# Kernel tuning notes

Measured on AMD Instinct MI355X. Metric: run time of the kernel, lower is better.

The kernel has to match this reference:

```python
import jax, jax.numpy as jnp
import numpy as np

N, C, T, H, W = 2, 512, 8, 28, 28
THW = T * H * W
BN_EPS = 1e-5


def conv1x1(x, Wt, b):
    # pointwise channel mixing, equivalent to 1x1 Conv2d/Conv3d on (N,C,T,H,W)
    return jnp.einsum('oc,ncthw->nothw', Wt, x) + b[None, :, None, None, None]


def setup_inputs() -> dict:
    key = jax.random.key(0)
    ks = jax.random.split(key, 8)
    s = 1.0 / np.sqrt(C)
    x = jax.random.normal(ks[0], (N, C, T, H, W), dtype=jnp.float32)
    mask = jax.random.uniform(ks[1], (N, C, T, H, W), dtype=jnp.float32)
    Wh = jax.random.normal(ks[2], (C, C), dtype=jnp.float32) * s
    Wg = jax.random.normal(ks[3], (C, C), dtype=jnp.float32) * s
    Wm = jax.random.normal(ks[4], (C, C), dtype=jnp.float32) * s
    Wz = jax.random.normal(ks[5], (C, C), dtype=jnp.float32) * s  # kaiming-like
    bh = jnp.zeros((C,), jnp.float32)
    bg = jnp.zeros((C,), jnp.float32)
    bm = jnp.zeros((C,), jnp.float32)
    bz = jnp.zeros((C,), jnp.float32)
    bn_w = jnp.ones((C,), jnp.float32)
    bn_b = jnp.zeros((C,), jnp.float32)
    gamma = jnp.float32(1.0)  # self.gamma (undefined in source __init__); learnable scalar
    return dict(x=x, mask=mask, Wh=Wh, bh=bh, Wg=Wg, bg=bg, Wm=Wm, bm=bm,
                Wz=Wz, bz=bz, bn_w=bn_w, bn_b=bn_b, gamma=gamma)


def reference(x, mask, Wh, bh, Wg, bg, Wm, bm, Wz, bz, bn_w, bn_b, gamma):
    n = x.shape[0]
    # proj_f = h(x) reshaped (N, THW, C); proj_g = g(x) (N, C, THW)
    ph_x = conv1x1(x, Wh, bh).reshape(n, C, THW)
    pg = conv1x1(x, Wg, bg).reshape(n, C, THW)
    # energy[n,t,s] = sum_c ph_x[n,c,t] * pg[n,c,s]  -> (N, THW, THW)
    energy = jnp.einsum('nct,ncs->nts', ph_x, pg)
    attention = jax.nn.softmax(energy, axis=-1)
    # proj_h uses self.h on mask (faithful to source)
    ph_m = conv1x1(mask, Wh, bh).reshape(n, C, THW)
    # bmm(proj_h, attention^T): [n,c,t] = sum_s ph_m[n,c,s] * attention[n,t,s]
    mask_energy = jnp.einsum('ncs,nts->nct', ph_m, attention)
    mask_atten = jax.nn.softmax(mask_energy, axis=-1)  # softmax over THW
    pm = conv1x1(x, Wm, bm)
    out = pm * mask_atten.reshape(n, C, T, H, W)
    # W_z: 1x1 Conv3d + BatchNorm3d (training-mode batch stats, weight=1, bias=0)
    wy = conv1x1(x, Wz, bz)
    mu = jnp.mean(wy, axis=(0, 2, 3, 4), keepdims=True)
    var = jnp.var(wy, axis=(0, 2, 3, 4), keepdims=True)
    wy = (wy - mu) * jax.lax.rsqrt(var + BN_EPS)
    wy = wy * bn_w[None, :, None, None, None] + bn_b[None, :, None, None, None]
    return gamma * out + wy
```

## Files before the change

### kernel.cpp

```cpp
#include <hip/hip_runtime.h>
#include <hip/hip_bf16.h>
#include <math.h>

#define NN 2
#define CC 512
#define PP 6272
#define TCHMAX 1664
#define NCHK 4
#define NJT 49
#define EM 64.0f
static const size_t PPC = (size_t)PP * CC;
static const size_t NCP = (size_t)NN * PPC;

typedef unsigned short ushortT;
typedef __attribute__((ext_vector_type(8))) short short8;
typedef __attribute__((ext_vector_type(4))) float f32x4;

__device__ __forceinline__ ushortT f2bf(float f) {
  __hip_bfloat16 h = __float2bfloat16(f);
  return *reinterpret_cast<ushortT*>(&h);
}
__device__ __forceinline__ float bf2f(ushortT u) {
  return __uint_as_float(((unsigned)u) << 16);
}

__device__ __forceinline__ void ld_g2l(const void* g, void* l) {
  __builtin_amdgcn_global_load_lds(
      (const __attribute__((address_space(1))) void*)g,
      (__attribute__((address_space(3))) void*)l, 16, 0, 0);
}

__device__ __forceinline__ int xcd_remap(int orig, int nwg) {
  const int q = nwg >> 3, r = nwg & 7;
  const int x = orig & 7, lo = orig >> 3;
  return (x < r) ? x * (q + 1) + lo : r * (q + 1) + (x - r) * q + lo;
}


__global__ __launch_bounds__(256) void k_cast4(const float* __restrict__ W0,
                                               const float* __restrict__ W1,
                                               const float* __restrict__ W2,
                                               const float* __restrict__ W3,
                                               ushortT* __restrict__ dst) {
  const float* src = (blockIdx.y == 0) ? W0 : (blockIdx.y == 1) ? W1
                    : (blockIdx.y == 2) ? W2 : W3;
  const int i = (blockIdx.x * 256 + threadIdx.x) * 4;
  float4 v = *(const float4*)&src[i];
  ushort4 o;
  o.x = f2bf(v.x); o.y = f2bf(v.y); o.z = f2bf(v.z); o.w = f2bf(v.w);
  *(ushort4*)&dst[(size_t)blockIdx.y * CC * CC + i] = o;
}

__global__ void k_castT2(const float* __restrict__ x,
                         const float* __restrict__ mask,
                         ushortT* __restrict__ xT,
                         ushortT* __restrict__ maskT) {
  __shared__ float T[32][33];
  const int zz = blockIdx.z;
  const float* in = (zz < 2) ? x : mask;
  ushortT* out = (zz < 2) ? xT : maskT;
  const int p0 = blockIdx.x * 32, c0 = blockIdx.y * 32;
  const int tx = threadIdx.x, ty = threadIdx.y;
  const size_t nbi = (size_t)(zz & 1) * PPC;
#pragma unroll
  for (int i = 0; i < 4; ++i)
    T[ty + i * 8][tx] = in[nbi + (size_t)(c0 + ty + i * 8) * PP + p0 + tx];
  __syncthreads();
#pragma unroll
  for (int i = 0; i < 4; ++i) {
    int r = ty + i * 8;
    out[nbi + (size_t)(p0 + r) * CC + c0 + tx] = f2bf(T[tx][r]);
  }
}

__global__ __launch_bounds__(256, 3) void k_convs(
    const ushortT* __restrict__ xT, const ushortT* __restrict__ maskT,
    const ushortT* __restrict__ Whbf, const ushortT* __restrict__ Wgbf,
    const ushortT* __restrict__ Wmbf, const ushortT* __restrict__ Wzbf,
    const float* __restrict__ bh, const float* __restrict__ bg,
    const float* __restrict__ bm, const float* __restrict__ bz,
    ushortT* __restrict__ phxT, ushortT* __restrict__ pgT,
    ushortT* __restrict__ phmB, ushortT* __restrict__ pmB,
    ushortT* __restrict__ wzb) {
  __shared__ __align__(16) ushortT smem[24576];
  const int tid = threadIdx.x;
  const int l = tid & 63, w = tid >> 6;
  const int orig = blockIdx.x;
  const int wgid = (orig & 7) * 147 + (orig >> 3);
  const int zq = wgid / 196;
  const int within = wgid % 196;
  const int ctile = within & 3;
  const int ptile = within >> 2;
  const int wA = (w & 1) * 64, wB = (w >> 1) * 64;
  const int lr = l & 15, lk = l >> 4;
  const int r4 = (l >> 4) * 4;
  const int srow = l >> 2;
  const int sg8 = ((l & 3) ^ ((l >> 3) & 3)) * 8;
  const int rg16 = (lk ^ ((lr >> 1) & 3)) * 16;

  int offL[4], offR[4];
#pragma unroll
  for (int t = 0; t < 4; ++t) {
    offL[t] = (wA + t * 16 + lr) * 64 + rg16;
    offR[t] = (wB + t * 16 + lr) * 64 + rg16;
  }

  auto stage = [&](const ushortT* src ,
                   ushortT* dst) {
#pragma unroll
    for (int i = 0; i < 2; ++i)
      ld_g2l(src + (size_t)(w * 32 + i * 16 + srow) * CC + sg8,
             (char*)dst + (w * 2 + i) * 1024);
  };
  auto ldf = [&](const ushortT* base, const int* off, short8* f) {
#pragma unroll
    for (int t = 0; t < 4; ++t)
      f[t] = *(const short8*)((const char*)base + off[t]);
  };

  ushortT* M0c = smem;          ushortT* M0n = smem + 4096;
  ushortT* M1c = smem + 8192;   ushortT* M1n = smem + 12288;
  ushortT* M2c = smem + 16384;  ushortT* M2n = smem + 20480;

  if (zq < 2) {
    const int zb = zq;
    const int p0 = ptile * 128, c0 = ctile * 128;
    const ushortT* Ax = xT + (size_t)zb * PPC + (size_t)p0 * CC;
    const ushortT* Bw1 = Whbf + (size_t)c0 * CC;
    const ushortT* Bw2 = Wgbf + (size_t)c0 * CC;
    ushortT* o1 = phxT + (size_t)zb * PPC;
    ushortT* o2 = pgT + (size_t)zb * PPC;
    f32x4 a1[4][4] = {}, a2[4][4] = {};
    stage(Ax, M0c); stage(Bw1, M1c); stage(Bw2, M2c);
    __syncthreads();
    for (int t = 0; t < 16; ++t) {
      if (t < 15) {
        const int k = (t + 1) * 32;
        stage(Ax + k, M0n); stage(Bw1 + k, M1n); stage(Bw2 + k, M2n);
      }
      short8 fp[4], fw[4];
      ldf(M0c, offL, fp);
      ldf(M1c, offR, fw);
#pragma unroll
      for (int ss = 0; ss < 4; ++ss)
#pragma unroll
        for (int tt = 0; tt < 4; ++tt)
          a1[ss][tt] = __builtin_amdgcn_mfma_f32_16x16x32_bf16(fw[ss], fp[tt], a1[ss][tt], 0, 0, 0);
      ldf(M2c, offR, fw);
#pragma unroll
      for (int ss = 0; ss < 4; ++ss)
#pragma unroll
        for (int tt = 0; tt < 4; ++tt)
          a2[ss][tt] = __builtin_amdgcn_mfma_f32_16x16x32_bf16(fw[ss], fp[tt], a2[ss][tt], 0, 0, 0);
      __syncthreads();
      ushortT* tp;
      tp = M0c; M0c = M0n; M0n = tp;
      tp = M1c; M1c = M1n; M1n = tp;
      tp = M2c; M2c = M2n; M2n = tp;
    }
#pragma unroll
    for (int tt = 0; tt < 4; ++tt) {
      const size_t prow = (size_t)(p0 + wA + tt * 16 + lr) * CC;
#pragma unroll
      for (int ss = 0; ss < 4; ++ss) {
        const int co = c0 + wB + ss * 16 + r4;
        float4 b1v = *(const float4*)&bh[co];
        float4 b2v = *(const float4*)&bg[co];
        ushort4 v1, v2;
        v1.x = f2bf(a1[ss][tt][0] + b1v.x);
        v1.y = f2bf(a1[ss][tt][1] + b1v.y);
        v1.z = f2bf(a1[ss][tt][2] + b1v.z);
        v1.w = f2bf(a1[ss][tt][3] + b1v.w);
        v2.x = f2bf(a2[ss][tt][0] + b2v.x);
        v2.y = f2bf(a2[ss][tt][1] + b2v.y);
        v2.z = f2bf(a2[ss][tt][2] + b2v.z);
        v2.w = f2bf(a2[ss][tt][3] + b2v.w);
        *(ushort4*)&o1[prow + co] = v1;
        *(ushort4*)&o2[prow + co] = v2;
      }
    }
  } else if (zq < 4) {
    const int zb = zq - 2;
    const int s0 = ptile * 128, c0 = ctile * 128;
    const ushortT* Am = maskT + (size_t)zb * PPC + (size_t)s0 * CC;
    const ushortT* Bw = Whbf + (size_t)c0 * CC;
    ushortT* o = phmB + (size_t)zb * PPC;
    f32x4 a[4][4] = {};
    stage(Am, M0c); stage(Bw, M1c);
    __syncthreads();
    for (int t = 0; t < 16; ++t) {
      if (t < 15) {
        const int k = (t + 1) * 32;
        stage(Am + k, M0n); stage(Bw + k, M1n);
      }
      short8 fs[4], fc[4];
      ldf(M0c, offL, fs);
      ldf(M1c, offR, fc);
#pragma unroll
      for (int ss = 0; ss < 4; ++ss)
#pragma unroll
        for (int tt = 0; tt < 4; ++tt)
          a[ss][tt] = __builtin_amdgcn_mfma_f32_16x16x32_bf16(fs[ss], fc[tt], a[ss][tt], 0, 0, 0);
      __syncthreads();
      ushortT* tp;
      tp = M0c; M0c = M0n; M0n = tp;
      tp = M1c; M1c = M1n; M1n = tp;
    }
#pragma unroll
    for (int tt = 0; tt < 4; ++tt) {
      const int c = c0 + wB + tt * 16 + lr;
      const float bi = bh[c];
      const size_t crow = (size_t)c * PP;
#pragma unroll
      for (int ss = 0; ss < 4; ++ss) {
        ushort4 v;
        v.x = f2bf(a[ss][tt][0] + bi);
        v.y = f2bf(a[ss][tt][1] + bi);
        v.z = f2bf(a[ss][tt][2] + bi);
        v.w = f2bf(a[ss][tt][3] + bi);
        *(ushort4*)&o[crow + s0 + wA + ss * 16 + r4] = v;
      }
    }
  } else {
    const int zb = zq - 4;
    const int p0 = ptile * 128, c0 = ctile * 128;
    const ushortT* Ax = xT + (size_t)zb * PPC + (size_t)p0 * CC;
    const ushortT* Bw1 = Wmbf + (size_t)c0 * CC;
    const ushortT* Bw2 = Wzbf + (size_t)c0 * CC;
    ushortT* o1 = pmB + (size_t)zb * PPC;
    ushortT* o2 = wzb + (size_t)zb * PPC;
    f32x4 a1[4][4] = {}, a2[4][4] = {};
    stage(Ax, M0c); stage(Bw1, M1c); stage(Bw2, M2c);
    __syncthreads();
    for (int t = 0; t < 16; ++t) {
      if (t < 15) {
        const int k = (t + 1) * 32;
        stage(Ax + k, M0n); stage(Bw1 + k, M1n); stage(Bw2 + k, M2n);
      }
      short8 fx[4], fw[4];
      ldf(M0c, offL, fx);
      ldf(M1c, offR, fw);
#pragma unroll
      for (int ss = 0; ss < 4; ++ss)
#pragma unroll
        for (int tt = 0; tt < 4; ++tt)
          a1[ss][tt] = __builtin_amdgcn_mfma_f32_16x16x32_bf16(fx[ss], fw[tt], a1[ss][tt], 0, 0, 0);
      ldf(M2c, offR, fw);
#pragma unroll
      for (int ss = 0; ss < 4; ++ss)
#pragma unroll
        for (int tt = 0; tt < 4; ++tt)
          a2[ss][tt] = __builtin_amdgcn_mfma_f32_16x16x32_bf16(fx[ss], fw[tt], a2[ss][tt], 0, 0, 0);
      __syncthreads();
      ushortT* tp;
      tp = M0c; M0c = M0n; M0n = tp;
      tp = M1c; M1c = M1n; M1n = tp;
      tp = M2c; M2c = M2n; M2n = tp;
    }
#pragma unroll
    for (int tt = 0; tt < 4; ++tt) {
      const int c = c0 + wB + tt * 16 + lr;
      const float b1v = bm[c], b2v = bz[c];
      const size_t crow = (size_t)c * PP;
#pragma unroll
      for (int ss = 0; ss < 4; ++ss) {
        const size_t off = crow + p0 + wA + ss * 16 + r4;
        ushort4 v1, v2;
        v1.x = f2bf(a1[ss][tt][0] + b1v);
        v1.y = f2bf(a1[ss][tt][1] + b1v);
        v1.z = f2bf(a1[ss][tt][2] + b1v);
        v1.w = f2bf(a1[ss][tt][3] + b1v);
        v2.x = f2bf(a2[ss][tt][0] + b2v);
        v2.y = f2bf(a2[ss][tt][1] + b2v);
        v2.z = f2bf(a2[ss][tt][2] + b2v);
        v2.w = f2bf(a2[ss][tt][3] + b2v);
        *(ushort4*)&o1[off] = v1;
        *(ushort4*)&o2[off] = v2;
      }
    }
  }
}

__global__ __launch_bounds__(256, 4) void k_energy(const ushortT* __restrict__ phxT,
                                                   const ushortT* __restrict__ pgT,
                                                   ushortT* __restrict__ Ech,
                                                   float* __restrict__ Estat,
                                                   int tbase) {
  __shared__ __align__(16) ushortT smem[16384];
  __shared__ float Ss[128][2];
  const int tid = threadIdx.x;
  const int l = tid & 63, w = tid >> 6;
  const int tiles = gridDim.y;
  const int orig = blockIdx.x + NJT * (blockIdx.y + tiles * blockIdx.z);
  const int wgid = xcd_remap(orig, NJT * tiles * NN);
  const int it = wgid % tiles;
  const int jt = (wgid / tiles) % NJT;
  const int z = wgid / (tiles * NJT);
  const int j0 = jt * 128;
  const int i0 = it * 128;
  const ushortT* Arow = phxT + (size_t)z * PPC + (size_t)(tbase + i0) * CC;
  const ushortT* Brow = pgT + (size_t)z * PPC + (size_t)j0 * CC;
  ushortT* out = Ech + (size_t)z * TCHMAX * PP;
  const int wi = (w & 1) * 64, wj = (w >> 1) * 64;
  const int lr = l & 15, lk = l >> 4;
  const int r4 = (l >> 4) * 4;
  const int srow = l >> 2;
  const int sg8 = ((l & 3) ^ ((l >> 3) & 3)) * 8;
  const int rg16 = (lk ^ ((lr >> 1) & 3)) * 16;

  int offA[4], offB[4];
#pragma unroll
  for (int t = 0; t < 4; ++t) {
    offA[t] = (wi + t * 16 + lr) * 64 + rg16;
    offB[t] = (wj + t * 16 + lr) * 64 + rg16;
  }
  auto stage = [&](const ushortT* src, ushortT* dst) {
#pragma unroll
    for (int i = 0; i < 2; ++i)
      ld_g2l(src + (size_t)(w * 32 + i * 16 + srow) * CC + sg8,
             (char*)dst + (w * 2 + i) * 1024);
  };

  ushortT* A0 = smem;          ushortT* A1 = smem + 4096;
  ushortT* B0 = smem + 8192;   ushortT* B1 = smem + 12288;

  f32x4 acc[4][4] = {};

  stage(Arow, A0); stage(Brow, B0);
  __syncthreads();
  ushortT *Ac = A0, *An = A1, *Bc = B0, *Bn = B1;
  for (int t = 0; t < 16; ++t) {
    if (t < 15) {
      const int k = (t + 1) * 32;
      stage(Arow + k, An); stage(Brow + k, Bn);
    }
    short8 af[4], bfv[4];
#pragma unroll
    for (int tt = 0; tt < 4; ++tt)
      af[tt] = *(const short8*)((const char*)Ac + offA[tt]);
#pragma unroll
    for (int ss = 0; ss < 4; ++ss)
      bfv[ss] = *(const short8*)((const char*)Bc + offB[ss]);
#pragma unroll
    for (int ss = 0; ss < 4; ++ss)
#pragma unroll
      for (int tt = 0; tt < 4; ++tt)
        acc[ss][tt] = __builtin_amdgcn_mfma_f32_16x16x32_bf16(bfv[ss], af[tt], acc[ss][tt], 0, 0, 0);
    __syncthreads();
    ushortT* tp;
    tp = Ac; Ac = An; An = tp;
    tp = Bc; Bc = Bn; Bn = tp;
  }
#pragma unroll
  for (int tt = 0; tt < 4; ++tt) {
    const int trow = i0 + wi + tt * 16 + lr;
    ushortT* orow = out + (size_t)trow * PP + j0;
    float sx = 0.f;
#pragma unroll
    for (int ss = 0; ss < 4; ++ss) {
      float u0 = __expf(acc[ss][tt][0] - EM);
      float u1 = __expf(acc[ss][tt][1] - EM);
      float u2 = __expf(acc[ss][tt][2] - EM);
      float u3 = __expf(acc[ss][tt][3] - EM);
      sx += (u0 + u1) + (u2 + u3);
      ushort4 v;
      v.x = f2bf(u0); v.y = f2bf(u1); v.z = f2bf(u2); v.w = f2bf(u3);
      *(ushort4*)&orow[wj + ss * 16 + r4] = v;
    }
    sx += __shfl_xor(sx, 16);
    sx += __shfl_xor(sx, 32);
    if (l < 16) Ss[wi + tt * 16 + l][w >> 1] = sx;
  }
  __syncthreads();
  if (tid < 128) {
    Estat[((size_t)z * TCHMAX + i0 + tid) * NJT + jt] = Ss[tid][0] + Ss[tid][1];
  }
}

__global__ __launch_bounds__(256) void k_zcomb(const float* __restrict__ Estat,
                                               float* __restrict__ rowZ, int rows) {
  const int r = blockIdx.x * 256 + threadIdx.x;
  if (r >= NN * rows) return;
  const int z = r / rows, tl = r % rows;
  const float* p = Estat + ((size_t)z * TCHMAX + tl) * NJT;
  float s = 0.f;
#pragma unroll
  for (int j = 0; j < NJT; ++j) s += p[j];
  rowZ[z * TCHMAX + tl] = 1.0f / s;
}

template <int KSPT>
__global__ __launch_bounds__(256, 6) void k_me(const ushortT* __restrict__ phmB,
                                               const ushortT* __restrict__ Ech,
                                               ushortT* __restrict__ mePart) {
  __shared__ __align__(16) ushortT smem[12288];
  const int tid = threadIdx.x;
  const int l = tid & 63, w = tid >> 6;
  const int gx = gridDim.x;
  const int orig = blockIdx.x + gx * (blockIdx.y + 4 * blockIdx.z);
  const int nwg = gx * 4 * (NN * KSPT);
  const int wgid = (orig & 7) * (nwg >> 3) + (orig >> 3);
  const int cb = wgid & 3;
  const int tl = (wgid >> 2) % gx;
  const int bz = (wgid >> 2) / gx;
  const int tl0 = tl * 64;
  const int c0 = cb * 128;
  const int z = bz / KSPT, ks = bz % KSPT;
  const ushortT* Arow = phmB + (size_t)z * PPC + (size_t)c0 * PP;
  const ushortT* Brow = Ech + (size_t)z * TCHMAX * PP + (size_t)tl0 * PP;
  const int wc = (w & 1) * 64, wt = (w >> 1) * 32;
  const int lr = l & 15, lk = l >> 4;
  const int r4 = (l >> 4) * 4;
  const int srow = l >> 2;
  const int sg8 = ((l & 3) ^ ((l >> 3) & 3)) * 8;
  const int rg16 = (lk ^ ((lr >> 1) & 3)) * 16;

  int offA[4], offB[2];
#pragma unroll
  for (int t = 0; t < 4; ++t) offA[t] = (wc + t * 16 + lr) * 64 + rg16;
#pragma unroll
  for (int t = 0; t < 2; ++t) offB[t] = (wt + t * 16 + lr) * 64 + rg16;

  auto stA = [&](const ushortT* src, ushortT* dst) {
#pragma unroll
    for (int i = 0; i < 2; ++i)
      ld_g2l(src + (size_t)(w * 32 + i * 16 + srow) * PP + sg8,
             (char*)dst + (w * 2 + i) * 1024);
  };
  auto stB = [&](const ushortT* src, ushortT* dst) {
    ld_g2l(src + (size_t)(w * 16 + srow) * PP + sg8, (char*)dst + w * 1024);
  };

  ushortT* A0 = smem;          ushortT* A1 = smem + 4096;
  ushortT* B0 = smem + 8192;   ushortT* B1 = smem + 10240;

  f32x4 acc[2][4] = {};

  const int sBeg = ((ks * 98) / KSPT) * 64;
  const int sEnd = (((ks + 1) * 98) / KSPT) * 64;
  const int NT = (sEnd - sBeg) >> 5;

  stA(Arow + sBeg, A0); stB(Brow + sBeg, B0);
  __syncthreads();
  ushortT *Ac = A0, *An = A1, *Bc = B0, *Bn = B1;
  for (int t = 0; t < NT; ++t) {
    if (t + 1 < NT) {
      const int k = sBeg + (t + 1) * 32;
      stA(Arow + k, An); stB(Brow + k, Bn);
    }
    short8 af[4], bfv[2];
#pragma unroll
    for (int ct = 0; ct < 4; ++ct)
      af[ct] = *(const short8*)((const char*)Ac + offA[ct]);
#pragma unroll
    for (int tt = 0; tt < 2; ++tt)
      bfv[tt] = *(const short8*)((const char*)Bc + offB[tt]);
#pragma unroll
    for (int tt = 0; tt < 2; ++tt)
#pragma unroll
      for (int ct = 0; ct < 4; ++ct)
        acc[tt][ct] = __builtin_amdgcn_mfma_f32_16x16x32_bf16(bfv[tt], af[ct], acc[tt][ct], 0, 0, 0);
    __syncthreads();
    ushortT* tp;
    tp = Ac; Ac = An; An = tp;
    tp = Bc; Bc = Bn; Bn = tp;
  }
  ushortT* out = mePart + ((size_t)(ks * NN + z) * CC) * TCHMAX;
#pragma unroll
  for (int ct = 0; ct < 4; ++ct) {
    const size_t crow = (size_t)(c0 + wc + ct * 16 + lr) * TCHMAX + tl0;
#pragma unroll
    for (int tt = 0; tt < 2; ++tt) {
      ushort4 v;
      v.x = f2bf(acc[tt][ct][0]);
      v.y = f2bf(acc[tt][ct][1]);
      v.z = f2bf(acc[tt][ct][2]);
      v.w = f2bf(acc[tt][ct][3]);
      *(ushort4*)&out[crow + wt + tt * 16 + r4] = v;
    }
  }
}

template <int KSPT>
__global__ __launch_bounds__(256) void k_meadd(const ushortT* __restrict__ mePart,
                                               const float* __restrict__ rowZ,
                                               ushortT* __restrict__ meb,
                                               int tbase, int rows) {
  const int idx = (blockIdx.x * 256 + threadIdx.x) * 4;
  const int tl = idx % rows;
  const int c = (idx / rows) % CC;
  const int z = idx / (rows * CC);
  float s0 = 0.f, s1 = 0.f, s2 = 0.f, s3 = 0.f;
#pragma unroll
  for (int ks = 0; ks < KSPT; ++ks) {
    const size_t o = ((size_t)(ks * NN + z) * CC + c) * TCHMAX + tl;
    ushort4 a = *(const ushort4*)&mePart[o];
    s0 += bf2f(a.x); s1 += bf2f(a.y); s2 += bf2f(a.z); s3 += bf2f(a.w);
  }
  const float4 rz = *(const float4*)&rowZ[z * TCHMAX + tl];
  ushort4 v;
  v.x = f2bf(s0 * rz.x); v.y = f2bf(s1 * rz.y);
  v.z = f2bf(s2 * rz.z); v.w = f2bf(s3 * rz.w);
  *(ushort4*)&meb[((size_t)z * CC + c) * PP + tbase + tl] = v;
}

__global__ __launch_bounds__(256) void k_soft2(const ushortT* __restrict__ me,
                                               float* __restrict__ m2,
                                               float* __restrict__ Z2) {
  __shared__ float red[256];
  const ushortT* row = me + (size_t)blockIdx.x * PP;
  const int tid = threadIdx.x;
  const int NCH = PP / 8;
  float m = -INFINITY;
  for (int i = tid; i < NCH; i += 256) {
    short8 v = *(const short8*)&row[i * 8];
#pragma unroll
    for (int j = 0; j < 8; ++j) m = fmaxf(m, bf2f((ushortT)v[j]));
  }
  red[tid] = m;
  __syncthreads();
  for (int s = 128; s > 0; s >>= 1) {
    if (tid < s) red[tid] = fmaxf(red[tid], red[tid + s]);
    __syncthreads();
  }
  m = red[0];
  __syncthreads();
  float zz = 0.f;
  for (int i = tid; i < NCH; i += 256) {
    short8 v = *(const short8*)&row[i * 8];
#pragma unroll
    for (int j = 0; j < 8; ++j) zz += __expf(bf2f((ushortT)v[j]) - m);
  }
  red[tid] = zz;
  __syncthreads();
  for (int s = 128; s > 0; s >>= 1) {
    if (tid < s) red[tid] += red[tid + s];
    __syncthreads();
  }
  if (tid == 0) { m2[blockIdx.x] = m; Z2[blockIdx.x] = red[0]; }
}

__global__ __launch_bounds__(256) void k_bnstat(const ushortT* __restrict__ wz,
                                                float* __restrict__ mu,
                                                float* __restrict__ rinv) {
  __shared__ float rs[256];
  __shared__ float rq[256];
  const int c = blockIdx.x;
  const int tid = threadIdx.x;
  const int NCH = PP / 8;
  float s = 0.f, q = 0.f;
  for (int n = 0; n < NN; ++n) {
    const ushortT* rowp = wz + (size_t)n * CC * PP + (size_t)c * PP;
    for (int i = tid; i < NCH; i += 256) {
      short8 v = *(const short8*)&rowp[i * 8];
#pragma unroll
      for (int j = 0; j < 8; ++j) {
        float f = bf2f((ushortT)v[j]);
        s += f;
        q += f * f;
      }
    }
  }
  rs[tid] = s; rq[tid] = q;
  __syncthreads();
  for (int st = 128; st > 0; st >>= 1) {
    if (tid < st) { rs[tid] += rs[tid + st]; rq[tid] += rq[tid + st]; }
    __syncthreads();
  }
  if (tid == 0) {
    const float inv_n = 1.0f / (float)(NN * PP);
    float mean = rs[0] * inv_n;
    float var = rq[0] * inv_n - mean * mean;
    mu[c] = mean;
    rinv[c] = rsqrtf(var + 1e-5f);
  }
}

__global__ __launch_bounds__(256) void k_final(const ushortT* __restrict__ pmB,
                                               const ushortT* __restrict__ me,
                                               const ushortT* __restrict__ wz,
                                               const float* __restrict__ m2,
                                               const float* __restrict__ Z2,
                                               const float* __restrict__ mu,
                                               const float* __restrict__ rinv,
                                               const float* __restrict__ bnw,
                                               const float* __restrict__ bnb,
                                               const float* __restrict__ gamma,
                                               float* __restrict__ out) {
  const int e4 = blockIdx.x * 256 + threadIdx.x;
  const size_t e = (size_t)e4 * 4;
  const int nc = (int)(e / PP);
  const int c = nc & (CC - 1);
  const float m = m2[nc];
  const float rz = 1.0f / Z2[nc];
  const float mub = mu[c];
  const float ri = rinv[c] * bnw[c];
  const float bb = bnb[c];
  const float g = gamma[0];
  ushort4 pv = *(const ushort4*)&pmB[e];
  ushort4 mev = *(const ushort4*)&me[e];
  ushort4 wzv = *(const ushort4*)&wz[e];
  float4 o;
  o.x = g * bf2f(pv.x) * (__expf(bf2f(mev.x) - m) * rz) + (bf2f(wzv.x) - mub) * ri + bb;
  o.y = g * bf2f(pv.y) * (__expf(bf2f(mev.y) - m) * rz) + (bf2f(wzv.y) - mub) * ri + bb;
  o.z = g * bf2f(pv.z) * (__expf(bf2f(mev.z) - m) * rz) + (bf2f(wzv.z) - mub) * ri + bb;
  o.w = g * bf2f(pv.w) * (__expf(bf2f(mev.w) - m) * rz) + (bf2f(wzv.w) - mub) * ri + bb;
  *(float4*)&out[e] = o;
}

extern "C" void kernel_launch(void* const* d_in, const int* in_sizes, int n_in,
                              void* d_out, int out_size, void* d_ws, size_t ws_size,
                              hipStream_t stream) {
  (void)in_sizes; (void)n_in; (void)out_size;
  const float* x    = (const float*)d_in[0];
  const float* mask = (const float*)d_in[1];
  const float* Wh   = (const float*)d_in[2];
  const float* bh   = (const float*)d_in[3];
  const float* Wg   = (const float*)d_in[4];
  const float* bg   = (const float*)d_in[5];
  const float* Wm   = (const float*)d_in[6];
  const float* bm   = (const float*)d_in[7];
  const float* Wz   = (const float*)d_in[8];
  const float* bz   = (const float*)d_in[9];
  const float* bnw  = (const float*)d_in[10];
  const float* bnb  = (const float*)d_in[11];
  const float* gam  = (const float*)d_in[12];

  ushortT* wzb  = (ushortT*)d_ws;
  ushortT* meb  = wzb + NCP;
  ushortT* pmB  = meb + NCP;
  ushortT* phxT = pmB + NCP;
  ushortT* pgT  = phxT + NCP;
  ushortT* phmB = pgT + NCP;
  ushortT* Wbf  = phmB + NCP;
  ushortT* Whbf = Wbf;
  ushortT* Wgbf = Wbf + 1 * CC * CC;
  ushortT* Wmbf = Wbf + 2 * CC * CC;
  ushortT* Wzbf = Wbf + 3 * CC * CC;
  float* m2    = (float*)(Wbf + 4 * CC * CC);
  float* Z2    = m2 + NN * CC;
  float* mu    = Z2 + NN * CC;
  float* rin   = mu + CC;
  float* Estat = rin + CC;
  float* rowZ  = Estat + (size_t)NN * TCHMAX * NJT;
  float* region = rowZ + (size_t)NN * TCHMAX + 16;
  ushortT* xT    = (ushortT*)region;
  ushortT* maskT = xT + NCP;
  ushortT* Ech    = (ushortT*)region;
  ushortT* mePart = Ech + (size_t)NN * TCHMAX * PP;

  const size_t regionOffB = (size_t)((char*)region - (char*)d_ws);
  const size_t need8 = regionOffB +
      ((size_t)NN * TCHMAX * PP + 8ull * NN * CC * TCHMAX) * 2;
  const bool k8 = ws_size >= need8;

  k_cast4<<<dim3(256, 4), 256, 0, stream>>>(Wh, Wg, Wm, Wz, Wbf);
  k_castT2<<<dim3(PP / 32, CC / 32, 4), dim3(32, 8), 0, stream>>>(x, mask, xT, maskT);

  k_convs<<<1176, 256, 0, stream>>>(xT, maskT, Whbf, Wgbf, Wmbf, Wzbf,
                                    bh, bg, bm, bz, phxT, pgT, phmB, pmB, wzb);

  static const int chunkTiles[NCHK] = {13, 12, 12, 12};
  int tbase = 0;
  for (int ch = 0; ch < NCHK; ++ch) {
    const int tiles = chunkTiles[ch];
    const int rows = tiles * 128;
    dim3 gE(NJT, tiles, NN);
    k_energy<<<gE, 256, 0, stream>>>(phxT, pgT, Ech, Estat, tbase);
    k_zcomb<<<(NN * rows + 255) / 256, 256, 0, stream>>>(Estat, rowZ, rows);
    if (k8) {
      dim3 gM(rows / 64, CC / 128, NN * 8);
      k_me<8><<<gM, 256, 0, stream>>>(phmB, Ech, mePart);
      k_meadd<8><<<NN * CC * rows / 1024, 256, 0, stream>>>(mePart, rowZ, meb,
                                                            tbase, rows);
    } else {
      dim3 gM(rows / 64, CC / 128, NN * 4);
      k_me<4><<<gM, 256, 0, stream>>>(phmB, Ech, mePart);
      k_meadd<4><<<NN * CC * rows / 1024, 256, 0, stream>>>(mePart, rowZ, meb,
                                                            tbase, rows);
    }
    tbase += rows;
  }

  k_soft2<<<NN * CC, 256, 0, stream>>>(meb, m2, Z2);
  k_bnstat<<<CC, 256, 0, stream>>>(wzb, mu, rin);
  const int total4 = (int)(NCP / 4);
  k_final<<<total4 / 256, 256, 0, stream>>>(pmB, meb, wzb, m2, Z2, mu, rin,
                                            bnw, bnb, gam, (float*)d_out);
}
```

Baseline: 579.9 us.

## Triple-buffer LDS staging with partial vmcnt waits in GEMM kernels

Converts the double-buffered global-to-LDS staging in k_convs, k_energy and k_me to a three-stage ring. Loads are now issued two K-steps ahead, and the full __syncthreads drain is replaced by a partial s_waitcnt vmcnt plus a raw barrier, so one stage of loads can stay in flight across the barrier. The MFMA blocks are also wrapped in s_setprio to favour math issue. The cost is more LDS per block and lower launch-bounds occupancy in all three kernels, and correctness now depends on the hand-counted vmcnt values matching the number of issued loads.

```diff
diff --git a/kernel.cpp b/kernel.cpp
--- a/kernel.cpp
+++ b/kernel.cpp
@@ -15,6 +15,9 @@
 typedef unsigned short ushortT;
 typedef __attribute__((ext_vector_type(8))) short short8;
 typedef __attribute__((ext_vector_type(4))) float f32x4;
+
+#define WAITV(N) asm volatile("s_waitcnt vmcnt(" #N ")" ::: "memory")
+#define BAR() __builtin_amdgcn_s_barrier()
 
 __device__ __forceinline__ ushortT f2bf(float f) {
   __hip_bfloat16 h = __float2bfloat16(f);
@@ -73,7 +76,7 @@
   }
 }
 
-__global__ __launch_bounds__(256, 3) void k_convs(
+__global__ __launch_bounds__(256, 2) void k_convs(
     const ushortT* __restrict__ xT, const ushortT* __restrict__ maskT,
     const ushortT* __restrict__ Whbf, const ushortT* __restrict__ Wgbf,
     const ushortT* __restrict__ Wmbf, const ushortT* __restrict__ Wzbf,
@@ -82,7 +85,7 @@
     ushortT* __restrict__ phxT, ushortT* __restrict__ pgT,
     ushortT* __restrict__ phmB, ushortT* __restrict__ pmB,
     ushortT* __restrict__ wzb) {
-  __shared__ __align__(16) ushortT smem[24576];
+  __shared__ __align__(16) ushortT smem[36864];
   const int tid = threadIdx.x;
   const int l = tid & 63, w = tid >> 6;
   const int orig = blockIdx.x;
@@ -105,8 +108,7 @@
     offR[t] = (wB + t * 16 + lr) * 64 + rg16;
   }
 
-  auto stage = [&](const ushortT* src ,
-                   ushortT* dst) {
+  auto stage = [&](const ushortT* src, ushortT* dst) {
 #pragma unroll
     for (int i = 0; i < 2; ++i)
       ld_g2l(src + (size_t)(w * 32 + i * 16 + srow) * CC + sg8,
@@ -118,9 +120,9 @@
       f[t] = *(const short8*)((const char*)base + off[t]);
   };
 
-  ushortT* M0c = smem;          ushortT* M0n = smem + 4096;
-  ushortT* M1c = smem + 8192;   ushortT* M1n = smem + 12288;
-  ushortT* M2c = smem + 16384;  ushortT* M2n = smem + 20480;
+  ushortT* Ca = smem;          ushortT* Na = smem + 4096;  ushortT* Za = smem + 8192;
+  ushortT* Cb = smem + 12288;  ushortT* Nb = smem + 16384; ushortT* Zb = smem + 20480;
+  ushortT* Cc = smem + 24576;  ushortT* Nc = smem + 28672; ushortT* Zc = smem + 32768;
 
   if (zq < 2) {
     const int zb = zq;
@@ -131,32 +133,38 @@
     ushortT* o1 = phxT + (size_t)zb * PPC;
     ushortT* o2 = pgT + (size_t)zb * PPC;
     f32x4 a1[4][4] = {}, a2[4][4] = {};
-    stage(Ax, M0c); stage(Bw1, M1c); stage(Bw2, M2c);
-    __syncthreads();
+    stage(Ax, Ca); stage(Bw1, Cb); stage(Bw2, Cc);
+    stage(Ax + 32, Na); stage(Bw1 + 32, Nb); stage(Bw2 + 32, Nc);
+    WAITV(6); BAR();
     for (int t = 0; t < 16; ++t) {
-      if (t < 15) {
-        const int k = (t + 1) * 32;
-        stage(Ax + k, M0n); stage(Bw1 + k, M1n); stage(Bw2 + k, M2n);
+      if (t < 14) {
+        const int k = (t + 2) * 32;
+        stage(Ax + k, Za); stage(Bw1 + k, Zb); stage(Bw2 + k, Zc);
       }
       short8 fp[4], fw[4];
-      ldf(M0c, offL, fp);
-      ldf(M1c, offR, fw);
+      ldf(Ca, offL, fp);
+      ldf(Cb, offR, fw);
+      __builtin_amdgcn_s_setprio(1);
 #pragma unroll
       for (int ss = 0; ss < 4; ++ss)
 #pragma unroll
         for (int tt = 0; tt < 4; ++tt)
           a1[ss][tt] = __builtin_amdgcn_mfma_f32_16x16x32_bf16(fw[ss], fp[tt], a1[ss][tt], 0, 0, 0);
-      ldf(M2c, offR, fw);
+      __builtin_amdgcn_s_setprio(0);
+      ldf(Cc, offR, fw);
+      __builtin_amdgcn_s_setprio(1);
 #pragma unroll
       for (int ss = 0; ss < 4; ++ss)
 #pragma unroll
         for (int tt = 0; tt < 4; ++tt)
           a2[ss][tt] = __builtin_amdgcn_mfma_f32_16x16x32_bf16(fw[ss], fp[tt], a2[ss][tt], 0, 0, 0);
-      __syncthreads();
+      __builtin_amdgcn_s_setprio(0);
+      if (t < 14) { WAITV(6); } else { WAITV(0); }
+      BAR();
       ushortT* tp;
-      tp = M0c; M0c = M0n; M0n = tp;
-      tp = M1c; M1c = M1n; M1n = tp;
-      tp = M2c; M2c = M2n; M2n = tp;
+      tp = Ca; Ca = Na; Na = Za; Za = tp;
+      tp = Cb; Cb = Nb; Nb = Zb; Zb = tp;
+      tp = Cc; Cc = Nc; Nc = Zc; Zc = tp;
     }
 #pragma unroll
     for (int tt = 0; tt < 4; ++tt) {
@@ -186,25 +194,29 @@
     const ushortT* Bw = Whbf + (size_t)c0 * CC;
     ushortT* o = phmB + (size_t)zb * PPC;
     f32x4 a[4][4] = {};
-    stage(Am, M0c); stage(Bw, M1c);
-    __syncthreads();
+    stage(Am, Ca); stage(Bw, Cb);
+    stage(Am + 32, Na); stage(Bw + 32, Nb);
+    WAITV(4); BAR();
     for (int t = 0; t < 16; ++t) {
-      if (t < 15) {
-        const int k = (t + 1) * 32;
-        stage(Am + k, M0n); stage(Bw + k, M1n);
+      if (t < 14) {
+        const int k = (t + 2) * 32;
+        stage(Am + k, Za); stage(Bw + k, Zb);
       }
       short8 fs[4], fc[4];
-      ldf(M0c, offL, fs);
-      ldf(M1c, offR, fc);
+      ldf(Ca, offL, fs);
+      ldf(Cb, offR, fc);
+      __builtin_amdgcn_s_setprio(1);
 #pragma unroll
       for (int ss = 0; ss < 4; ++ss)
 #pragma unroll
         for (int tt = 0; tt < 4; ++tt)
           a[ss][tt] = __builtin_amdgcn_mfma_f32_16x16x32_bf16(fs[ss], fc[tt], a[ss][tt], 0, 0, 0);
-      __syncthreads();
+      __builtin_amdgcn_s_setprio(0);
+      if (t < 14) { WAITV(4); } else { WAITV(0); }
+      BAR();
       ushortT* tp;
-      tp = M0c; M0c = M0n; M0n = tp;
-      tp = M1c; M1c = M1n; M1n = tp;
+      tp = Ca; Ca = Na; Na = Za; Za = tp;
+      tp = Cb; Cb = Nb; Nb = Zb; Zb = tp;
     }
 #pragma unroll
     for (int tt = 0; tt < 4; ++tt) {
@@ -230,32 +242,38 @@
     ushortT* o1 = pmB + (size_t)zb * PPC;
     ushortT* o2 = wzb + (size_t)zb * PPC;
     f32x4 a1[4][4] = {}, a2[4][4] = {};
-    stage(Ax, M0c); stage(Bw1, M1c); stage(Bw2, M2c);
-    __syncthreads();
+    stage(Ax, Ca); stage(Bw1, Cb); stage(Bw2, Cc);
+    stage(Ax + 32, Na); stage(Bw1 + 32, Nb); stage(Bw2 + 32, Nc);
+    WAITV(6); BAR();
     for (int t = 0; t < 16; ++t) {
-      if (t < 15) {
-        const int k = (t + 1) * 32;
-        stage(Ax + k, M0n); stage(Bw1 + k, M1n); stage(Bw2 + k, M2n);
+      if (t < 14) {
+        const int k = (t + 2) * 32;
+        stage(Ax + k, Za); stage(Bw1 + k, Zb); stage(Bw2 + k, Zc);
       }
       short8 fx[4], fw[4];
-      ldf(M0c, offL, fx);
-      ldf(M1c, offR, fw);
+      ldf(Ca, offL, fx);
+      ldf(Cb, offR, fw);
+      __builtin_amdgcn_s_setprio(1);
 #pragma unroll
       for (int ss = 0; ss < 4; ++ss)
 #pragma unroll
         for (int tt = 0; tt < 4; ++tt)
           a1[ss][tt] = __builtin_amdgcn_mfma_f32_16x16x32_bf16(fx[ss], fw[tt], a1[ss][tt], 0, 0, 0);
-      ldf(M2c, offR, fw);
+      __builtin_amdgcn_s_setprio(0);
+      ldf(Cc, offR, fw);
+      __builtin_amdgcn_s_setprio(1);
 #pragma unroll
       for (int ss = 0; ss < 4; ++ss)
 #pragma unroll
         for (int tt = 0; tt < 4; ++tt)
           a2[ss][tt] = __builtin_amdgcn_mfma_f32_16x16x32_bf16(fx[ss], fw[tt], a2[ss][tt], 0, 0, 0);
-      __syncthreads();
+      __builtin_amdgcn_s_setprio(0);
+      if (t < 14) { WAITV(6); } else { WAITV(0); }
+      BAR();
       ushortT* tp;
-      tp = M0c; M0c = M0n; M0n = tp;
-      tp = M1c; M1c = M1n; M1n = tp;
-      tp = M2c; M2c = M2n; M2n = tp;
+      tp = Ca; Ca = Na; Na = Za; Za = tp;
+      tp = Cb; Cb = Nb; Nb = Zb; Zb = tp;
+      tp = Cc; Cc = Nc; Nc = Zc; Zc = tp;
     }
 #pragma unroll
     for (int tt = 0; tt < 4; ++tt) {
@@ -281,12 +299,12 @@
   }
 }
 
-__global__ __launch_bounds__(256, 4) void k_energy(const ushortT* __restrict__ phxT,
+__global__ __launch_bounds__(256, 3) void k_energy(const ushortT* __restrict__ phxT,
                                                    const ushortT* __restrict__ pgT,
                                                    ushortT* __restrict__ Ech,
                                                    float* __restrict__ Estat,
                                                    int tbase) {
-  __shared__ __align__(16) ushortT smem[16384];
+  __shared__ __align__(16) ushortT smem[24576];
   __shared__ float Ss[128][2];
   const int tid = threadIdx.x;
   const int l = tid & 63, w = tid >> 6;
@@ -321,18 +339,18 @@
              (char*)dst + (w * 2 + i) * 1024);
   };
 
-  ushortT* A0 = smem;          ushortT* A1 = smem + 4096;
-  ushortT* B0 = smem + 8192;   ushortT* B1 = smem + 12288;
+  ushortT* Ac = smem;          ushortT* An = smem + 4096;  ushortT* Az = smem + 8192;
+  ushortT* Bc = smem + 12288;  ushortT* Bn = smem + 16384; ushortT* Bz = smem + 20480;
 
   f32x4 acc[4][4] = {};
 
-  stage(Arow, A0); stage(Brow, B0);
-  __syncthreads();
-  ushortT *Ac = A0, *An = A1, *Bc = B0, *Bn = B1;
+  stage(Arow, Ac); stage(Brow, Bc);
+  stage(Arow + 32, An); stage(Brow + 32, Bn);
+  WAITV(4); BAR();
   for (int t = 0; t < 16; ++t) {
-    if (t < 15) {
-      const int k = (t + 1) * 32;
-      stage(Arow + k, An); stage(Brow + k, Bn);
+    if (t < 14) {
+      const int k = (t + 2) * 32;
+      stage(Arow + k, Az); stage(Brow + k, Bz);
     }
     short8 af[4], bfv[4];
 #pragma unroll
@@ -341,15 +359,18 @@
 #pragma unroll
     for (int ss = 0; ss < 4; ++ss)
       bfv[ss] = *(const short8*)((const char*)Bc + offB[ss]);
+    __builtin_amdgcn_s_setprio(1);
 #pragma unroll
     for (int ss = 0; ss < 4; ++ss)
 #pragma unroll
       for (int tt = 0; tt < 4; ++tt)
         acc[ss][tt] = __builtin_amdgcn_mfma_f32_16x16x32_bf16(bfv[ss], af[tt], acc[ss][tt], 0, 0, 0);
-    __syncthreads();
+    __builtin_amdgcn_s_setprio(0);
+    if (t < 14) { WAITV(4); } else { WAITV(0); }
+    BAR();
     ushortT* tp;
-    tp = Ac; Ac = An; An = tp;
-    tp = Bc; Bc = Bn; Bn = tp;
+    tp = Ac; Ac = An; An = Az; Az = tp;
+    tp = Bc; Bc = Bn; Bn = Bz; Bz = tp;
   }
 #pragma unroll
   for (int tt = 0; tt < 4; ++tt) {
@@ -390,10 +411,10 @@
 }
 
 template <int KSPT>
-__global__ __launch_bounds__(256, 6) void k_me(const ushortT* __restrict__ phmB,
+__global__ __launch_bounds__(256, 4) void k_me(const ushortT* __restrict__ phmB,
                                                const ushortT* __restrict__ Ech,
                                                ushortT* __restrict__ mePart) {
-  __shared__ __align__(16) ushortT smem[12288];
+  __shared__ __align__(16) ushortT smem[18432];
   const int tid = threadIdx.x;
   const int l = tid & 63, w = tid >> 6;
   const int gx = gridDim.x;
@@ -431,8 +452,8 @@
     ld_g2l(src + (size_t)(w * 16 + srow) * PP + sg8, (char*)dst + w * 1024);
   };
 
-  ushortT* A0 = smem;          ushortT* A1 = smem + 4096;
-  ushortT* B0 = smem + 8192;   ushortT* B1 = smem + 10240;
+  ushortT* Ac = smem;          ushortT* An = smem + 4096;  ushortT* Az = smem + 8192;
+  ushortT* Bc = smem + 12288;  ushortT* Bn = smem + 14336; ushortT* Bz = smem + 16384;
 
   f32x4 acc[2][4] = {};
 
@@ -440,13 +461,13 @@
   const int sEnd = (((ks + 1) * 98) / KSPT) * 64;
   const int NT = (sEnd - sBeg) >> 5;
 
-  stA(Arow + sBeg, A0); stB(Brow + sBeg, B0);
-  __syncthreads();
-  ushortT *Ac = A0, *An = A1, *Bc = B0, *Bn = B1;
+  stA(Arow + sBeg, Ac); stB(Brow + sBeg, Bc);
+  stA(Arow + sBeg + 32, An); stB(Brow + sBeg + 32, Bn);
+  WAITV(3); BAR();
   for (int t = 0; t < NT; ++t) {
-    if (t + 1 < NT) {
-      const int k = sBeg + (t + 1) * 32;
-      stA(Arow + k, An); stB(Brow + k, Bn);
+    if (t + 2 < NT) {
+      const int k = sBeg + (t + 2) * 32;
+      stA(Arow + k, Az); stB(Brow + k, Bz);
     }
     short8 af[4], bfv[2];
 #pragma unroll
@@ -455,15 +476,18 @@
 #pragma unroll
     for (int tt = 0; tt < 2; ++tt)
       bfv[tt] = *(const short8*)((const char*)Bc + offB[tt]);
+    __builtin_amdgcn_s_setprio(1);
 #pragma unroll
     for (int tt = 0; tt < 2; ++tt)
 #pragma unroll
       for (int ct = 0; ct < 4; ++ct)
         acc[tt][ct] = __builtin_amdgcn_mfma_f32_16x16x32_bf16(bfv[tt], af[ct], acc[tt][ct], 0, 0, 0);
-    __syncthreads();
+    __builtin_amdgcn_s_setprio(0);
+    if (t + 2 < NT) { WAITV(3); } else { WAITV(0); }
+    BAR();
     ushortT* tp;
-    tp = Ac; Ac = An; An = tp;
-    tp = Bc; Bc = Bn; Bn = tp;
+    tp = Ac; Ac = An; An = Az; Az = tp;
+    tp = Bc; Bc = Bn; Bn = Bz; Bz = tp;
   }
   ushortT* out = mePart + ((size_t)(ks * NN + z) * CC) * TCHMAX;
 #pragma unroll
```

Result: faster. 548.1 us (-5.5%).
